# Kernel tuning notes

Measured on AMD Instinct MI355X. Metric: run time of the kernel, lower is better.

## Reference

```python
import jax, jax.numpy as jnp
import numpy as np

SCALE = 8.0  # cfg.TEST_SCALE (eval path)


def setup_inputs() -> dict:
    key = jax.random.key(0)
    ks = jax.random.split(key, 5)
    N, D, F, NC = 65536, 1024, 300, 81
    return {
        "x": jax.random.normal(ks[0], (N, D), dtype=jnp.float32),
        "W_cls": jax.random.normal(ks[1], (1, D), dtype=jnp.float32) * 0.01,
        "b_cls": jnp.zeros((1,), dtype=jnp.float32),
        "W_sem": jax.random.normal(ks[2], (F, D), dtype=jnp.float32) * 0.01,
        "b_sem": jnp.zeros((F,), dtype=jnp.float32),
        "W_bbox": jax.random.normal(ks[3], (NC * 4, D), dtype=jnp.float32) * 0.001,
        "b_bbox": jnp.zeros((NC * 4,), dtype=jnp.float32),
        "sem_matrix": jax.random.normal(ks[4], (NC - 1, F), dtype=jnp.float32),
    }


def reference(x, W_cls, b_cls, W_sem, b_sem, W_bbox, b_bbox, sem_matrix):
    # b_score: Linear(D, 1)
    b_score = x @ W_cls.T + b_cls                      # [N, 1]
    # sem: Linear(D, F)
    sem = x @ W_sem.T + b_sem                          # [N, F]
    # eval path: scale * L2-row-normalized semantic matrix
    sm = SCALE * sem_matrix / jnp.linalg.norm(sem_matrix, axis=1, keepdims=True)
    # the original per-class repeat/mul/sum loop == one GEMM
    cls_score = sem @ sm.T                             # [N, NC-1]
    scores = jnp.concatenate([b_score, cls_score], axis=1)  # [N, NC]
    bbox_deltas = x @ W_bbox.T + b_bbox                # [N, NC*4]
    return (scores, bbox_deltas)
```

## Files before the change

kernel.cpp:

```cpp
#include <hip/hip_runtime.h>
#include <hip/hip_bf16.h>
#include <stdint.h>

#define KDIM 1024
#define NPAD 416
#define NCOLS 405
#define SCORE_COLS 81
#define BBOX_COLS 324
#define NROWS 65536
#define FDIM 300
#define SLAB (NPAD * 32)


typedef short v8s __attribute__((ext_vector_type(8)));
typedef float v4f __attribute__((ext_vector_type(4)));

__device__ __forceinline__ uint16_t f2bf(float f) {
    union { float f; uint32_t u; } c; c.f = f;
    uint32_t r = c.u + 0x7FFFu + ((c.u >> 16) & 1u);
    return (uint16_t)(r >> 16);
}

__device__ __forceinline__ size_t wt_off(int row, int k) {
    return (size_t)(k >> 5) * SLAB + (size_t)row * 32 + (k & 31);
}

__global__ void fill_w(const float* __restrict__ Wcls, const float* __restrict__ bcls,
                       const float* __restrict__ Wbbox, const float* __restrict__ bbbox,
                       uint16_t* __restrict__ Wt, float* __restrict__ bt) {
    int idx = blockIdx.x * 256 + threadIdx.x;
    int row = idx >> 10, k = idx & 1023;
    if (!(row >= 1 && row < 81)) {
        float v;
        if (row == 0) v = Wcls[k];
        else if (row < 81 + BBOX_COLS) v = Wbbox[(size_t)(row - 81) * KDIM + k];
        else v = 0.f;
        Wt[wt_off(row, k)] = f2bf(v);
    }
    if (k == 0 && !(row >= 1 && row < 81)) {
        float b;
        if (row == 0) b = bcls[0];
        else if (row < 81 + BBOX_COLS) b = bbbox[row - 81];
        else b = 0.f;
        bt[row] = b;
    }
}

__global__ void fill_w_sem(const float* __restrict__ Wsem, const float* __restrict__ bsem,
                           const float* __restrict__ semm,
                           uint16_t* __restrict__ Wt, float* __restrict__ bt) {
    const int n = blockIdx.x;
    const int kq = blockIdx.y;
    const int tid = threadIdx.x;
    __shared__ float s_row[FDIM];
    __shared__ float red[256];
    __shared__ float s_scale, s_bdot;

    const float* sr = semm + (size_t)n * FDIM;
    float p = 0.f, pb = 0.f;
    for (int f = tid; f < FDIM; f += 256) {
        float v = sr[f];
        s_row[f] = v;
        p += v * v;
        pb += v * bsem[f];
    }
    red[tid] = p; __syncthreads();
    for (int s = 128; s > 0; s >>= 1) { if (tid < s) red[tid] += red[tid + s]; __syncthreads(); }
    float norm2 = red[0]; __syncthreads();
    red[tid] = pb; __syncthreads();
    for (int s = 128; s > 0; s >>= 1) { if (tid < s) red[tid] += red[tid + s]; __syncthreads(); }
    if (tid == 0) { s_scale = 8.0f / sqrtf(norm2); s_bdot = red[0]; }
    __syncthreads();
    const float scale = s_scale;
    if (kq == 0 && tid == 0) bt[1 + n] = scale * s_bdot;

    const int k = kq * 256 + tid;
    float acc = 0.f;
    #pragma unroll 8
    for (int f = 0; f < FDIM; ++f) acc += s_row[f] * Wsem[(size_t)f * KDIM + k];
    Wt[wt_off(1 + n, k)] = f2bf(scale * acc);
}

#define A_STRIDE 36
#define A_BUF_ELEMS (64 * A_STRIDE)
#define EPS_STRIDE 409
#define SMEM_BYTES (32 * EPS_STRIDE * 4)

__device__ __forceinline__ void stcvt(uint16_t* p, float4 av) {
    __hip_bfloat162 lo = __float22bfloat162_rn(make_float2(av.x, av.y));
    __hip_bfloat162 hi = __float22bfloat162_rn(make_float2(av.z, av.w));
    uint2 v; v.x = *(uint32_t*)&lo; v.y = *(uint32_t*)&hi;
    *(uint2*)p = v;
}

__global__ __launch_bounds__(512, 4) void gemm_fused(
        const float* __restrict__ x, const uint16_t* __restrict__ Wt,
        const float* __restrict__ bt, float* __restrict__ out) {
    const int tid = threadIdx.x;
    const int wave = tid >> 6, lane = tid & 63;
    const int quad = lane >> 4, l16 = lane & 15;
    const int mtile = blockIdx.x;
    const int NT = (wave < 6) ? 4 : (wave == 6 ? 2 : 0);

    __shared__ __align__(16) char smem[SMEM_BYTES];
    uint16_t* As = (uint16_t*)smem;

    const float* xb = x + (size_t)mtile * 64 * KDIM;
    const int colbase = wave * 64;

    v4f acc[4][4];
    #pragma unroll
    for (int mi = 0; mi < 4; ++mi)
        #pragma unroll
        for (int ni = 0; ni < 4; ++ni)
            acc[mi][ni] = v4f{0.f, 0.f, 0.f, 0.f};

    const int am = tid >> 3, akc = tid & 7;
    const float* aptr = xb + (size_t)am * KDIM + akc * 4;
    const uint16_t* bptr = Wt + (size_t)(colbase + l16) * 32 + quad * 8;

    v8s bcur[4];

    float4 av0  = *(const float4*)aptr;
    float4 av_n = *(const float4*)(aptr + 32);
    #pragma unroll
    for (int ni = 0; ni < 4; ++ni)
        if (ni < NT) bcur[ni] = *(const v8s*)(bptr + ni * 512);
    stcvt(As + am * A_STRIDE + akc * 4, av0);
    asm volatile("s_waitcnt lgkmcnt(0)" ::: "memory");
    __builtin_amdgcn_s_barrier();
    asm volatile("" ::: "memory");

    int rb = 0, wb = 1;
    float4 av_nn;
    for (int kt = 0; kt < 32; ++kt) {
        if (kt < 30) av_nn = *(const float4*)(aptr + (size_t)(kt + 2) * 32);
        const uint16_t* Ar = As + rb * A_BUF_ELEMS;
        v8s a0 = *(const v8s*)(Ar + (0 * 16 + l16) * A_STRIDE + quad * 8);
        v8s a1 = *(const v8s*)(Ar + (1 * 16 + l16) * A_STRIDE + quad * 8);
        v8s a2 = *(const v8s*)(Ar + (2 * 16 + l16) * A_STRIDE + quad * 8);
        v8s a3 = *(const v8s*)(Ar + (3 * 16 + l16) * A_STRIDE + quad * 8);
        const uint16_t* bnext = bptr + (size_t)(kt + 1) * SLAB;
        #pragma unroll
        for (int ni = 0; ni < 4; ++ni) {
            if (ni < NT) {
                acc[0][ni] = __builtin_amdgcn_mfma_f32_16x16x32_bf16(a0, bcur[ni], acc[0][ni], 0, 0, 0);
                acc[1][ni] = __builtin_amdgcn_mfma_f32_16x16x32_bf16(a1, bcur[ni], acc[1][ni], 0, 0, 0);
                acc[2][ni] = __builtin_amdgcn_mfma_f32_16x16x32_bf16(a2, bcur[ni], acc[2][ni], 0, 0, 0);
                acc[3][ni] = __builtin_amdgcn_mfma_f32_16x16x32_bf16(a3, bcur[ni], acc[3][ni], 0, 0, 0);
                if (kt < 31) bcur[ni] = *(const v8s*)(bnext + ni * 512);
            }
        }
        if (kt < 31) {
            stcvt(As + wb * A_BUF_ELEMS + am * A_STRIDE + akc * 4, av_n);
            av_n = av_nn;
            asm volatile("s_waitcnt lgkmcnt(0)" ::: "memory");
            __builtin_amdgcn_s_barrier();
            asm volatile("" ::: "memory");
            int ib = 3 - rb - wb; rb = wb; wb = ib;
        }
    }

    const int rowbase = mtile * 64;
    float* eps = (float*)smem;
    float* outb = out + (size_t)NROWS * SCORE_COLS;
    float bias[4];
    #pragma unroll
    for (int ni = 0; ni < 4; ++ni)
        bias[ni] = (ni < NT) ? bt[colbase + ni * 16 + l16] : 0.f;
    #pragma unroll
    for (int h = 0; h < 2; ++h) {
        __syncthreads();
        #pragma unroll
        for (int mi2 = 0; mi2 < 2; ++mi2) {
            const int mi = h * 2 + mi2;
            #pragma unroll
            for (int ni = 0; ni < 4; ++ni) {
                const int col = colbase + ni * 16 + l16;
                if (ni < NT && col < NCOLS) {
                    #pragma unroll
                    for (int r = 0; r < 4; ++r)
                        eps[(mi2 * 16 + quad * 4 + r) * EPS_STRIDE + col] = acc[mi][ni][r] + bias[ni];
                }
            }
        }
        __syncthreads();
        const int row0 = rowbase + h * 32;
        for (int idx = tid; idx < 32 * SCORE_COLS; idx += 512) {
            int r = idx / SCORE_COLS, c = idx - r * SCORE_COLS;
            __builtin_nontemporal_store(eps[r * EPS_STRIDE + c],
                                        &out[(size_t)(row0 + r) * SCORE_COLS + c]);
        }
        for (int idx = tid; idx < 32 * BBOX_COLS; idx += 512) {
            int r = idx / BBOX_COLS, c = idx - r * BBOX_COLS;
            __builtin_nontemporal_store(eps[r * EPS_STRIDE + SCORE_COLS + c],
                                        &outb[(size_t)(row0 + r) * BBOX_COLS + c]);
        }
    }
}

extern "C" void kernel_launch(void* const* d_in, const int* in_sizes, int n_in,
                              void* d_out, int out_size, void* d_ws, size_t ws_size,
                              hipStream_t stream) {
    const float* x     = (const float*)d_in[0];
    const float* Wcls  = (const float*)d_in[1];
    const float* bcls  = (const float*)d_in[2];
    const float* Wsem  = (const float*)d_in[3];
    const float* bsem  = (const float*)d_in[4];
    const float* Wbbox = (const float*)d_in[5];
    const float* bbbox = (const float*)d_in[6];
    const float* semm  = (const float*)d_in[7];
    float* out = (float*)d_out;

    uint16_t* Wt = (uint16_t*)d_ws;
    float*    bt = (float*)((char*)d_ws + (size_t)NPAD * KDIM * 2);

    fill_w<<<dim3((NPAD * KDIM) / 256), dim3(256), 0, stream>>>(Wcls, bcls, Wbbox, bbbox, Wt, bt);
    fill_w_sem<<<dim3(80, 4), dim3(256), 0, stream>>>(Wsem, bsem, semm, Wt, bt);
    gemm_fused<<<dim3(NROWS / 64), dim3(512), 0, stream>>>(x, Wt, bt, out);
}
```

Before: 493.5 us.

## Load A fragments directly from global into registers and interleave column tiles across waves

Drops the LDS staging of the x tile, its double buffering and the per-step barriers. Each wave now loads and converts its own A fragments straight from global memory into MFMA registers. Column tiles are assigned round-robin (wave + 8*ni), so every wave does 3 or 4 tiles instead of some waves doing none. The cost is that all 8 waves each read the full 64x1024 fp32 x tile and convert it to bf16 redundantly, relying on L1/L2 to absorb the extra global traffic.

```diff
diff --git a/kernel.cpp b/kernel.cpp
--- a/kernel.cpp
+++ b/kernel.cpp
@@ -81,16 +81,18 @@
     Wt[wt_off(1 + n, k)] = f2bf(scale * acc);
 }
 
-#define A_STRIDE 36
-#define A_BUF_ELEMS (64 * A_STRIDE)
 #define EPS_STRIDE 409
 #define SMEM_BYTES (32 * EPS_STRIDE * 4)
 
-__device__ __forceinline__ void stcvt(uint16_t* p, float4 av) {
-    __hip_bfloat162 lo = __float22bfloat162_rn(make_float2(av.x, av.y));
-    __hip_bfloat162 hi = __float22bfloat162_rn(make_float2(av.z, av.w));
-    uint2 v; v.x = *(uint32_t*)&lo; v.y = *(uint32_t*)&hi;
-    *(uint2*)p = v;
+__device__ __forceinline__ v8s pack8(float4 f0, float4 f1) {
+    __hip_bfloat162 p0 = __float22bfloat162_rn(make_float2(f0.x, f0.y));
+    __hip_bfloat162 p1 = __float22bfloat162_rn(make_float2(f0.z, f0.w));
+    __hip_bfloat162 p2 = __float22bfloat162_rn(make_float2(f1.x, f1.y));
+    __hip_bfloat162 p3 = __float22bfloat162_rn(make_float2(f1.z, f1.w));
+    union { v8s v; uint32_t u[4]; } r;
+    r.u[0] = *(uint32_t*)&p0; r.u[1] = *(uint32_t*)&p1;
+    r.u[2] = *(uint32_t*)&p2; r.u[3] = *(uint32_t*)&p3;
+    return r.v;
 }
 
 __global__ __launch_bounds__(512, 4) void gemm_fused(
@@ -100,13 +102,9 @@
     const int wave = tid >> 6, lane = tid & 63;
     const int quad = lane >> 4, l16 = lane & 15;
     const int mtile = blockIdx.x;
-    const int NT = (wave < 6) ? 4 : (wave == 6 ? 2 : 0);
+    const bool four = (wave < 2);
 
     __shared__ __align__(16) char smem[SMEM_BYTES];
-    uint16_t* As = (uint16_t*)smem;
-
-    const float* xb = x + (size_t)mtile * 64 * KDIM;
-    const int colbase = wave * 64;
 
     v4f acc[4][4];
     #pragma unroll
@@ -115,59 +113,58 @@
         for (int ni = 0; ni < 4; ++ni)
             acc[mi][ni] = v4f{0.f, 0.f, 0.f, 0.f};
 
-    const int am = tid >> 3, akc = tid & 7;
-    const float* aptr = xb + (size_t)am * KDIM + akc * 4;
-    const uint16_t* bptr = Wt + (size_t)(colbase + l16) * 32 + quad * 8;
+    const float* ap = x + ((size_t)(mtile * 64 + l16)) * KDIM + quad * 8;
+
+    const uint16_t* bfrag[4];
+    #pragma unroll
+    for (int ni = 0; ni < 4; ++ni) {
+        int t = wave + 8 * ni; if (t > 25) t = 25;
+        bfrag[ni] = Wt + (size_t)(t * 16 + l16) * 32 + quad * 8;
+    }
 
     v8s bcur[4];
-
-    float4 av0  = *(const float4*)aptr;
-    float4 av_n = *(const float4*)(aptr + 32);
-    #pragma unroll
-    for (int ni = 0; ni < 4; ++ni)
-        if (ni < NT) bcur[ni] = *(const v8s*)(bptr + ni * 512);
-    stcvt(As + am * A_STRIDE + akc * 4, av0);
-    asm volatile("s_waitcnt lgkmcnt(0)" ::: "memory");
-    __builtin_amdgcn_s_barrier();
-    asm volatile("" ::: "memory");
-
-    int rb = 0, wb = 1;
-    float4 av_nn;
+    bcur[0] = *(const v8s*)bfrag[0];
+    bcur[1] = *(const v8s*)bfrag[1];
+    bcur[2] = *(const v8s*)bfrag[2];
+    bcur[3] = four ? *(const v8s*)bfrag[3] : v8s{0, 0, 0, 0, 0, 0, 0, 0};
+
     for (int kt = 0; kt < 32; ++kt) {
-        if (kt < 30) av_nn = *(const float4*)(aptr + (size_t)(kt + 2) * 32);
-        const uint16_t* Ar = As + rb * A_BUF_ELEMS;
-        v8s a0 = *(const v8s*)(Ar + (0 * 16 + l16) * A_STRIDE + quad * 8);
-        v8s a1 = *(const v8s*)(Ar + (1 * 16 + l16) * A_STRIDE + quad * 8);
-        v8s a2 = *(const v8s*)(Ar + (2 * 16 + l16) * A_STRIDE + quad * 8);
-        v8s a3 = *(const v8s*)(Ar + (3 * 16 + l16) * A_STRIDE + quad * 8);
-        const uint16_t* bnext = bptr + (size_t)(kt + 1) * SLAB;
-        #pragma unroll
-        for (int ni = 0; ni < 4; ++ni) {
-            if (ni < NT) {
-                acc[0][ni] = __builtin_amdgcn_mfma_f32_16x16x32_bf16(a0, bcur[ni], acc[0][ni], 0, 0, 0);
-                acc[1][ni] = __builtin_amdgcn_mfma_f32_16x16x32_bf16(a1, bcur[ni], acc[1][ni], 0, 0, 0);
-                acc[2][ni] = __builtin_amdgcn_mfma_f32_16x16x32_bf16(a2, bcur[ni], acc[2][ni], 0, 0, 0);
-                acc[3][ni] = __builtin_amdgcn_mfma_f32_16x16x32_bf16(a3, bcur[ni], acc[3][ni], 0, 0, 0);
-                if (kt < 31) bcur[ni] = *(const v8s*)(bnext + ni * 512);
-            }
-        }
-        if (kt < 31) {
-            stcvt(As + wb * A_BUF_ELEMS + am * A_STRIDE + akc * 4, av_n);
-            av_n = av_nn;
-            asm volatile("s_waitcnt lgkmcnt(0)" ::: "memory");
-            __builtin_amdgcn_s_barrier();
-            asm volatile("" ::: "memory");
-            int ib = 3 - rb - wb; rb = wb; wb = ib;
+        v8s a[4];
+        #pragma unroll
+        for (int mi = 0; mi < 4; ++mi) {
+            const float* p = ap + (size_t)mi * 16 * KDIM + kt * 32;
+            float4 f0 = *(const float4*)p;
+            float4 f1 = *(const float4*)(p + 4);
+            a[mi] = pack8(f0, f1);
+        }
+        const size_t nxt = (size_t)((kt + 1) & 31) * SLAB;
+        #pragma unroll
+        for (int ni = 0; ni < 3; ++ni) {
+            acc[0][ni] = __builtin_amdgcn_mfma_f32_16x16x32_bf16(a[0], bcur[ni], acc[0][ni], 0, 0, 0);
+            acc[1][ni] = __builtin_amdgcn_mfma_f32_16x16x32_bf16(a[1], bcur[ni], acc[1][ni], 0, 0, 0);
+            acc[2][ni] = __builtin_amdgcn_mfma_f32_16x16x32_bf16(a[2], bcur[ni], acc[2][ni], 0, 0, 0);
+            acc[3][ni] = __builtin_amdgcn_mfma_f32_16x16x32_bf16(a[3], bcur[ni], acc[3][ni], 0, 0, 0);
+            bcur[ni] = *(const v8s*)(bfrag[ni] + nxt);
+        }
+        if (four) {
+            acc[0][3] = __builtin_amdgcn_mfma_f32_16x16x32_bf16(a[0], bcur[3], acc[0][3], 0, 0, 0);
+            acc[1][3] = __builtin_amdgcn_mfma_f32_16x16x32_bf16(a[1], bcur[3], acc[1][3], 0, 0, 0);
+            acc[2][3] = __builtin_amdgcn_mfma_f32_16x16x32_bf16(a[2], bcur[3], acc[2][3], 0, 0, 0);
+            acc[3][3] = __builtin_amdgcn_mfma_f32_16x16x32_bf16(a[3], bcur[3], acc[3][3], 0, 0, 0);
+            bcur[3] = *(const v8s*)(bfrag[3] + nxt);
         }
     }
 
     const int rowbase = mtile * 64;
     float* eps = (float*)smem;
     float* outb = out + (size_t)NROWS * SCORE_COLS;
+    const int NT = four ? 4 : 3;
     float bias[4];
     #pragma unroll
-    for (int ni = 0; ni < 4; ++ni)
-        bias[ni] = (ni < NT) ? bt[colbase + ni * 16 + l16] : 0.f;
+    for (int ni = 0; ni < 4; ++ni) {
+        const int col = (wave + 8 * ni) * 16 + l16;
+        bias[ni] = (ni < NT) ? bt[col <= 415 ? col : 0] : 0.f;
+    }
     #pragma unroll
     for (int h = 0; h < 2; ++h) {
         __syncthreads();
@@ -176,7 +173,7 @@
             const int mi = h * 2 + mi2;
             #pragma unroll
             for (int ni = 0; ni < 4; ++ni) {
-                const int col = colbase + ni * 16 + l16;
+                const int col = (wave + 8 * ni) * 16 + l16;
                 if (ni < NT && col < NCOLS) {
                     #pragma unroll
                     for (int r = 0; r < 4; ++r)
```

New measurement: 637.8 us. +29.2%, slower.
